# Optimization experiments

Measured on AMD Instinct MI355X. Metric: run time of the kernel, lower is better.

Reference implementation:

```python
import jax, jax.numpy as jnp
import numpy as np

N = 100_000      # nodes
E = 1_600_000    # edges (avg degree 16)
D = 128          # emb_dim == hidden_dim
OUT = 128        # out_dim
NUM_BOND_TYPE = 6
NUM_BOND_DIR = 3


def _xavier(key, fan_in, fan_out, shape):
    a = np.sqrt(6.0 / (fan_in + fan_out)).astype(np.float32)
    return jax.random.uniform(key, shape, jnp.float32, -a, a)


def setup_inputs() -> dict:
    key = jax.random.key(0)
    ks = jax.random.split(key, 12)
    x = jax.random.normal(ks[0], (N, D), jnp.float32)
    edge_index = jax.random.randint(ks[1], (2, E), 0, N)
    edge_attr = jax.random.randint(ks[2], (E, 2), 0, NUM_BOND_DIR)
    # PReLU single learnable slope (torch init 0.25)
    prelu_a = jnp.full((1,), 0.25, jnp.float32)
    # enc_to_dec: Linear(D, D, bias=False), torch default uniform(-1/sqrt(D), 1/sqrt(D))
    s = 1.0 / np.sqrt(D)
    W_enc = jax.random.uniform(ks[3], (D, D), jnp.float32, -s, s)
    # edge embedding tables, xavier_uniform
    emb1 = _xavier(ks[4], NUM_BOND_TYPE, D, (NUM_BOND_TYPE, D))
    emb2 = _xavier(ks[5], NUM_BOND_DIR, D, (NUM_BOND_DIR, D))
    # GIN MLP: Linear(D, 2D) -> ReLU -> Linear(2D, OUT)
    W1 = jax.random.uniform(ks[6], (2 * D, D), jnp.float32, -s, s)
    b1 = jax.random.uniform(ks[7], (2 * D,), jnp.float32, -s, s)
    s2 = 1.0 / np.sqrt(2 * D)
    W2 = jax.random.uniform(ks[8], (OUT, 2 * D), jnp.float32, -s2, s2)
    b2 = jax.random.uniform(ks[9], (OUT,), jnp.float32, -s2, s2)
    return {
        "x": x, "edge_index": edge_index, "edge_attr": edge_attr,
        "prelu_a": prelu_a, "W_enc": W_enc,
        "emb1": emb1, "emb2": emb2,
        "W1": W1, "b1": b1, "W2": W2, "b2": b2,
    }


def reference(x, edge_index, edge_attr, prelu_a, W_enc, emb1, emb2, W1, b1, W2, b2):
    # PReLU then enc_to_dec (no bias)
    h = jnp.where(x >= 0, x, prelu_a * x)          # [N, D]
    h = h @ W_enc.T                                 # [N, D]
    src, dst = edge_index[0], edge_index[1]
    # edge embeddings for real edges
    e_emb = emb1[edge_attr[:, 0]] + emb2[edge_attr[:, 1]]  # [E, D]
    # messages: x_j + edge_attr, scatter-add at dst
    msg = h[src] + e_emb                             # [E, D]
    agg = jax.ops.segment_sum(msg, dst, num_segments=N)    # [N, D]
    # self-loops: appended edge (i, i) with attr [4, 0]
    self_emb = emb1[4] + emb2[0]                     # [D]
    agg = agg + h + self_emb[None, :]
    # GIN update MLP
    hid = jax.nn.relu(agg @ W1.T + b1)               # [N, 2D]
    out = hid @ W2.T + b2                            # [N, OUT]
    return out
```

## Files before the change

kernel.cpp:

```cpp
#include <hip/hip_runtime.h>
#include <hip/hip_bf16.h>

#define DD 128

typedef short bf16x8 __attribute__((ext_vector_type(8)));
typedef float f32x4 __attribute__((ext_vector_type(4)));

__device__ __forceinline__ float bf2f_lo(unsigned int u) {
    union { unsigned int v; float f; } x; x.v = u << 16; return x.f;
}
__device__ __forceinline__ float bf2f_hi(unsigned int u) {
    union { unsigned int v; float f; } x; x.v = u & 0xFFFF0000u; return x.f;
}
__device__ __forceinline__ unsigned short f2bf(float f) {
    union { float f; unsigned int u; } x; x.f = f;
    unsigned int u = x.u;
    unsigned int r = (u + 0x7FFFu + ((u >> 16) & 1u)) >> 16;
    return (unsigned short)r;
}

__global__ __launch_bounds__(256) void wcvt_k(const float* __restrict__ Wenc,
                                              const float* __restrict__ W1,
                                              const float* __restrict__ W2,
                                              unsigned short* __restrict__ wb) {
    int i = (blockIdx.x * 256 + threadIdx.x) * 4;
    if (i >= 81920) return;
    const float* src;
    int off;
    if (i < 16384)      { src = Wenc; off = 0; }
    else if (i < 49152) { src = W1;   off = 16384; }
    else                { src = W2;   off = 49152; }
    float4 v = *(const float4*)&src[i - off];
    ushort4 w;
    w.x = f2bf(v.x); w.y = f2bf(v.y); w.z = f2bf(v.z); w.w = f2bf(v.w);
    *(ushort4*)&wb[i] = w;
}

__global__ __launch_bounds__(256) void gemm1_k(
    const float* __restrict__ Ap, const unsigned short* __restrict__ Wb,
    unsigned short* __restrict__ Hb,
    const float* __restrict__ prelu_a, int M)
{
    const int K = 128;
    const int tid = threadIdx.x;
    const int wid = tid >> 6, lane = tid & 63;
    const float pa = prelu_a[0];

    const int r0 = blockIdx.x * 128 + wid * 32;
    const int rl = lane & 15, kb = (lane >> 4) * 8;

    bf16x8 af[2][4];
    #pragma unroll
    for (int rf = 0; rf < 2; ++rf) {
        int row = r0 + rf * 16 + rl; if (row > M - 1) row = M - 1;
        #pragma unroll
        for (int kf = 0; kf < 4; ++kf) {
            float4 v0 = *(const float4*)&Ap[(size_t)row * K + kf * 32 + kb];
            float4 v1 = *(const float4*)&Ap[(size_t)row * K + kf * 32 + kb + 4];
            v0.x = v0.x >= 0.f ? v0.x : pa * v0.x;
            v0.y = v0.y >= 0.f ? v0.y : pa * v0.y;
            v0.z = v0.z >= 0.f ? v0.z : pa * v0.z;
            v0.w = v0.w >= 0.f ? v0.w : pa * v0.w;
            v1.x = v1.x >= 0.f ? v1.x : pa * v1.x;
            v1.y = v1.y >= 0.f ? v1.y : pa * v1.y;
            v1.z = v1.z >= 0.f ? v1.z : pa * v1.z;
            v1.w = v1.w >= 0.f ? v1.w : pa * v1.w;
            bf16x8 t;
            t[0] = (short)f2bf(v0.x); t[1] = (short)f2bf(v0.y);
            t[2] = (short)f2bf(v0.z); t[3] = (short)f2bf(v0.w);
            t[4] = (short)f2bf(v1.x); t[5] = (short)f2bf(v1.y);
            t[6] = (short)f2bf(v1.z); t[7] = (short)f2bf(v1.w);
            af[rf][kf] = t;
        }
    }

    f32x4 acc[8][2];
    const f32x4 zz = {0.f, 0.f, 0.f, 0.f};
    #pragma unroll
    for (int nt = 0; nt < 8; ++nt) { acc[nt][0] = zz; acc[nt][1] = zz; }

    #pragma unroll
    for (int nt = 0; nt < 8; ++nt) {
        bf16x8 bf[4];
        #pragma unroll
        for (int kf = 0; kf < 4; ++kf)
            bf[kf] = *(const bf16x8*)&Wb[(size_t)(nt * 16 + rl) * K + kf * 32 + kb];
        #pragma unroll
        for (int rf = 0; rf < 2; ++rf)
            #pragma unroll
            for (int kf = 0; kf < 4; ++kf)
                acc[nt][rf] = __builtin_amdgcn_mfma_f32_16x16x32_bf16(af[rf][kf], bf[kf], acc[nt][rf], 0, 0, 0);
    }

    const int rq = (lane >> 4) * 4;
    #pragma unroll
    for (int nt = 0; nt < 8; ++nt) {
        int c = nt * 16 + rl;
        #pragma unroll
        for (int rf = 0; rf < 2; ++rf) {
            int rb = r0 + rf * 16 + rq;
            #pragma unroll
            for (int t = 0; t < 4; ++t) {
                int r = rb + t;
                if (r < M) Hb[(size_t)r * 128 + c] = f2bf(acc[nt][rf][t]);
            }
        }
    }
}

__global__ __launch_bounds__(512) void mlp_k(
    const unsigned short* __restrict__ A,
    const unsigned short* __restrict__ w1b,
    const float* __restrict__ b1,
    const unsigned short* __restrict__ w2b,
    const float* __restrict__ b2,
    float* __restrict__ out, int M)
{
    __shared__ unsigned short W1l[256][136];
    __shared__ unsigned short hidl[128][264];
    unsigned short (*W2l)[264] = (unsigned short (*)[264])&W1l[0][0];

    const int tid = threadIdx.x;
    const int wid = tid >> 6, lane = tid & 63;
    const int rl = lane & 15, kb = (lane >> 4) * 8;
    const int rq = (lane >> 4) * 4;
    const int r0 = blockIdx.x * 128;

    #pragma unroll
    for (int idx = tid; idx < 256 * 16; idx += 512) {
        int n = idx >> 4, kq = idx & 15;
        *(ushort4*)&W1l[n][kq * 8] = *(const ushort4*)&w1b[(size_t)n * 128 + kq * 8];
        *(ushort4*)&W1l[n][kq * 8 + 4] = *(const ushort4*)&w1b[(size_t)n * 128 + kq * 8 + 4];
    }
    bf16x8 af[4];
    {
        int row = r0 + wid * 16 + rl; if (row > M - 1) row = M - 1;
        #pragma unroll
        for (int kf = 0; kf < 4; ++kf)
            af[kf] = *(const bf16x8*)&A[(size_t)row * 128 + kf * 32 + kb];
    }
    __syncthreads();

    f32x4 acc1[16];
    const f32x4 zz = {0.f, 0.f, 0.f, 0.f};
    #pragma unroll
    for (int nt = 0; nt < 16; ++nt) acc1[nt] = zz;
    #pragma unroll
    for (int nt = 0; nt < 16; ++nt) {
        bf16x8 bf[4];
        #pragma unroll
        for (int kf = 0; kf < 4; ++kf)
            bf[kf] = *(const bf16x8*)&W1l[nt * 16 + rl][kf * 32 + kb];
        #pragma unroll
        for (int kf = 0; kf < 4; ++kf)
            acc1[nt] = __builtin_amdgcn_mfma_f32_16x16x32_bf16(af[kf], bf[kf], acc1[nt], 0, 0, 0);
    }
    #pragma unroll
    for (int nt = 0; nt < 16; ++nt) {
        int c = nt * 16 + rl;
        float bi = b1[c];
        #pragma unroll
        for (int t = 0; t < 4; ++t)
            hidl[wid * 16 + rq + t][c] = f2bf(fmaxf(acc1[nt][t] + bi, 0.f));
    }
    __syncthreads();

    #pragma unroll
    for (int idx = tid; idx < 128 * 32; idx += 512) {
        int n = idx >> 5, kq = idx & 31;
        *(ushort4*)&W2l[n][kq * 8] = *(const ushort4*)&w2b[(size_t)n * 256 + kq * 8];
        *(ushort4*)&W2l[n][kq * 8 + 4] = *(const ushort4*)&w2b[(size_t)n * 256 + kq * 8 + 4];
    }
    __syncthreads();

    bf16x8 af2[8];
    #pragma unroll
    for (int kf = 0; kf < 8; ++kf)
        af2[kf] = *(const bf16x8*)&hidl[wid * 16 + rl][kf * 32 + kb];
    f32x4 acc2[8];
    #pragma unroll
    for (int nt = 0; nt < 8; ++nt) acc2[nt] = zz;
    #pragma unroll
    for (int nt = 0; nt < 8; ++nt) {
        bf16x8 bf[8];
        #pragma unroll
        for (int kf = 0; kf < 8; ++kf)
            bf[kf] = *(const bf16x8*)&W2l[nt * 16 + rl][kf * 32 + kb];
        #pragma unroll
        for (int kf = 0; kf < 8; ++kf)
            acc2[nt] = __builtin_amdgcn_mfma_f32_16x16x32_bf16(af2[kf], bf[kf], acc2[nt], 0, 0, 0);
    }
    #pragma unroll
    for (int nt = 0; nt < 8; ++nt) {
        int c = nt * 16 + rl;
        float bi = b2[c];
        #pragma unroll
        for (int t = 0; t < 4; ++t) {
            int r = r0 + wid * 16 + rq + t;
            if (r < M) out[(size_t)r * 128 + c] = acc2[nt][t] + bi;
        }
    }
}


#define SBSH 10
#define SBN  1024
#define NBP 128

__global__ __launch_bounds__(256) void sbhist_k(const int* __restrict__ ei,
                                                int* __restrict__ bh,
                                                int E, int chunk, int nsb) {
    __shared__ int h4[4][128];
    int wid = threadIdx.x >> 6;
    for (int i = threadIdx.x; i < 4 * 128; i += 256) ((int*)h4)[i] = 0;
    __syncthreads();
    int b = blockIdx.x;
    int beg = b * chunk, end = min(E, beg + chunk);
    for (int e = beg + threadIdx.x; e < end; e += 256)
        atomicAdd(&h4[wid][ei[E + e] >> SBSH], 1);
    __syncthreads();
    for (int i = threadIdx.x; i < nsb; i += 256)
        bh[i * NBP + b] = h4[0][i] + h4[1][i] + h4[2][i] + h4[3][i];
}

__global__ __launch_bounds__(1024) void sbscan_k(const int* __restrict__ bh,
                                                 int* __restrict__ bho,
                                                 int ntot, int* __restrict__ offs,
                                                 int M, int E) {
    __shared__ int ws[16];
    int tid = threadIdx.x;
    int ch = (ntot + 1023) / 1024;
    int beg = tid * ch, end = min(ntot, beg + ch);
    int s = 0;
    for (int i = beg; i < end; ++i) s += bh[i];
    int lane = tid & 63, wid = tid >> 6;
    int ss = s;
    #pragma unroll
    for (int o = 1; o < 64; o <<= 1) { int t = __shfl_up(ss, o, 64); if (lane >= o) ss += t; }
    if (lane == 63) ws[wid] = ss;
    __syncthreads();
    if (tid == 0) { int c = 0; for (int w = 0; w < 16; ++w) { int t = ws[w]; ws[w] = c; c += t; } }
    __syncthreads();
    int excl = ss - s + ws[wid];
    for (int i = beg; i < end; ++i) { int t = bh[i]; bho[i] = excl; excl += t; }
    if (tid == 0) offs[M] = E;
}

__global__ __launch_bounds__(256) void part_k(const int* __restrict__ ei,
                                              const int* __restrict__ ea,
                                              const int* __restrict__ bho,
                                              int* __restrict__ rec,
                                              int E, int chunk, int nsb) {
    __shared__ int cur[128];
    int b = blockIdx.x;
    for (int i = threadIdx.x; i < nsb; i += 256) cur[i] = bho[i * NBP + b];
    __syncthreads();
    int beg = b * chunk, end = min(E, beg + chunk);
    for (int e = beg + threadIdx.x; e < end; e += 256) {
        int src = ei[e];
        int dst = ei[E + e];
        int2 aa = *(const int2*)&ea[2 * e];
        int pos = atomicAdd(&cur[dst >> SBSH], 1);
        rec[pos] = src | ((aa.x * 3 + aa.y) << 17) | ((dst & (SBN - 1)) << 21);
    }
}

__global__ __launch_bounds__(1024) void csr_k(const int* __restrict__ rec,
                                              const int* __restrict__ bho,
                                              int* __restrict__ offs,
                                              int* __restrict__ packed,
                                              int nsb, int M, int E) {
    __shared__ int hist[SBN];
    __shared__ int lstart[SBN];
    __shared__ int wsum[16];
    int s = blockIdx.x;
    int t = threadIdx.x;
    int sb0 = bho[s * NBP];
    int sb1 = (s == nsb - 1) ? E : bho[(s + 1) * NBP];
    hist[t] = 0;
    __syncthreads();
    for (int i = sb0 + t; i < sb1; i += 1024)
        atomicAdd(&hist[(rec[i] >> 21) & (SBN - 1)], 1);
    __syncthreads();
    int v = hist[t];
    int lane = t & 63, wid = t >> 6;
    int ss = v;
    #pragma unroll
    for (int o = 1; o < 64; o <<= 1) { int u = __shfl_up(ss, o, 64); if (lane >= o) ss += u; }
    if (lane == 63) wsum[wid] = ss;
    __syncthreads();
    if (t == 0) { int c = 0; for (int w = 0; w < 16; ++w) { int x = wsum[w]; wsum[w] = c; c += x; } }
    __syncthreads();
    int excl = ss - v + wsum[wid];
    lstart[t] = excl;
    int node = (s << SBSH) + t;
    if (node < M) offs[node] = sb0 + excl;
    hist[t] = 0;
    __syncthreads();
    for (int i = sb0 + t; i < sb1; i += 1024) {
        int r = rec[i];
        int dl = (r >> 21) & (SBN - 1);
        int pos = sb0 + lstart[dl] + atomicAdd(&hist[dl], 1);
        packed[pos] = r & 0x1FFFFF;
    }
}

__global__ __launch_bounds__(256) void agg_k(const unsigned short* __restrict__ h,
                                             const int* __restrict__ packed,
                                             const int* __restrict__ offs,
                                             const float* __restrict__ emb1,
                                             const float* __restrict__ emb2,
                                             unsigned int* __restrict__ aggb, int M) {
    __shared__ float emb12[10][DD];
    for (int t = threadIdx.x; t < 10 * DD; t += 256) {
        int c = t >> 7, col = t & 127;
        float v;
        if (c == 9) v = emb1[4 * DD + col] + emb2[col];
        else        v = emb1[(c / 3) * DD + col] + emb2[(c % 3) * DD + col];
        emb12[c][col] = v;
    }
    __syncthreads();
    int wid = threadIdx.x >> 6, lane = threadIdx.x & 63;
    int n = blockIdx.x * 4 + wid;
    if (n >= M) return;
    n = __builtin_amdgcn_readfirstlane(n);
    int c2 = lane * 2;
    int beg = offs[n], end = offs[n + 1];
    unsigned int hn = *(const unsigned int*)&h[(size_t)n * DD + c2];
    float2 se = *(const float2*)&emb12[9][c2];
    float2 acc = {bf2f_lo(hn) + se.x, bf2f_hi(hn) + se.y};
    int e = beg;
    for (; e + 8 <= end; e += 8) {
        int p[8]; unsigned int hv[8]; float2 m[8];
        #pragma unroll
        for (int i = 0; i < 8; ++i) p[i] = packed[e + i];
        #pragma unroll
        for (int i = 0; i < 8; ++i)
            hv[i] = *(const unsigned int*)&h[(size_t)(p[i] & 0x1FFFF) * DD + c2];
        #pragma unroll
        for (int i = 0; i < 8; ++i)
            m[i] = *(const float2*)&emb12[(p[i] >> 17) & 15][c2];
        #pragma unroll
        for (int i = 0; i < 8; ++i) {
            acc.x += bf2f_lo(hv[i]) + m[i].x;
            acc.y += bf2f_hi(hv[i]) + m[i].y;
        }
    }
    if (e + 4 <= end) {
        int p[4]; unsigned int hv[4]; float2 m[4];
        #pragma unroll
        for (int i = 0; i < 4; ++i) p[i] = packed[e + i];
        #pragma unroll
        for (int i = 0; i < 4; ++i)
            hv[i] = *(const unsigned int*)&h[(size_t)(p[i] & 0x1FFFF) * DD + c2];
        #pragma unroll
        for (int i = 0; i < 4; ++i)
            m[i] = *(const float2*)&emb12[(p[i] >> 17) & 15][c2];
        #pragma unroll
        for (int i = 0; i < 4; ++i) {
            acc.x += bf2f_lo(hv[i]) + m[i].x;
            acc.y += bf2f_hi(hv[i]) + m[i].y;
        }
        e += 4;
    }
    for (; e < end; ++e) {
        int p = packed[e];
        unsigned int hv = *(const unsigned int*)&h[(size_t)(p & 0x1FFFF) * DD + c2];
        float2 m = *(const float2*)&emb12[(p >> 17) & 15][c2];
        acc.x += bf2f_lo(hv) + m.x;
        acc.y += bf2f_hi(hv) + m.y;
    }
    aggb[((size_t)n * DD + c2) >> 1] = ((unsigned int)f2bf(acc.y) << 16) | f2bf(acc.x);
}

extern "C" void kernel_launch(void* const* d_in, const int* in_sizes, int n_in,
                              void* d_out, int out_size, void* d_ws, size_t ws_size,
                              hipStream_t stream) {
    const float* x     = (const float*)d_in[0];
    const int*   ei    = (const int*)d_in[1];
    const int*   ea    = (const int*)d_in[2];
    const float* pa    = (const float*)d_in[3];
    const float* Wenc  = (const float*)d_in[4];
    const float* emb1  = (const float*)d_in[5];
    const float* emb2  = (const float*)d_in[6];
    const float* W1    = (const float*)d_in[7];
    const float* b1    = (const float*)d_in[8];
    const float* W2    = (const float*)d_in[9];
    const float* b2    = (const float*)d_in[10];
    float* out = (float*)d_out;

    const int M = in_sizes[0] / DD;
    const int E = in_sizes[1] / 2;
    const int nsb = (M + SBN - 1) >> SBSH;
    const int chunk = (E + NBP - 1) / NBP;

    char* ws = (char*)d_ws;
    size_t o = 0;
    unsigned short* h_bf  = (unsigned short*)(ws + o); o += (size_t)M * DD * 2;
    unsigned int*   aggb  = (unsigned int*)(ws + o);   o += (size_t)M * DD * 2;
    int* rec    = (int*)(ws + o); o += (size_t)E * 4;
    int* packed = (int*)(ws + o); o += (size_t)E * 4;
    int* offs   = (int*)(ws + o); o += (size_t)(M + 1) * 4;
    int* bh     = (int*)(ws + o); o += (size_t)nsb * NBP * 4;
    int* bho    = (int*)(ws + o); o += (size_t)nsb * NBP * 4;
    unsigned short* wb = (unsigned short*)(ws + o); o += 81920 * 2;
    unsigned short* wenc_b = wb;
    unsigned short* w1_b   = wb + 16384;
    unsigned short* w2_b   = wb + 49152;

    dim3 blk(256);

    wcvt_k<<<dim3(80), blk, 0, stream>>>(Wenc, W1, W2, wb);

    sbhist_k<<<dim3(NBP), blk, 0, stream>>>(ei, bh, E, chunk, nsb);
    sbscan_k<<<dim3(1), dim3(1024), 0, stream>>>(bh, bho, nsb * NBP, offs, M, E);
    part_k<<<dim3(NBP), blk, 0, stream>>>(ei, ea, bho, rec, E, chunk, nsb);
    csr_k<<<dim3(nsb), dim3(1024), 0, stream>>>(rec, bho, offs, packed, nsb, M, E);

    gemm1_k<<<dim3((M + 127) / 128), blk, 0, stream>>>(x, wenc_b, h_bf, pa, M);

    agg_k<<<dim3((M + 3) / 4), blk, 0, stream>>>(h_bf, packed, offs, emb1, emb2, aggb, M);

    mlp_k<<<dim3((M + 127) / 128), dim3(512), 0, stream>>>(
        (const unsigned short*)aggb, w1_b, b1, w2_b, b2, out, M);
}
```

Measured before the change: 223.9 us.

## Fuse histogram, weight convert and GEMM1; merge CSR build into aggregation

Merges the destination histogram, the W1/W2 bf16 conversion and the PReLU+enc GEMM into one heterogeneous launch, with Wenc converted inline from fp32 inside each GEMM block. The CSR local sort is fused with aggregation, so each super-bucket block sorts its edges and then aggregates its own nodes without a global offsets array. Super-buckets shrink from 1024 to 128 nodes and the partition block count from 128 to 64. This cuts launches and a global round trip through the offsets array, at the cost of more scan entries, redundant Wenc conversion in every GEMM block, and smaller aggregation grids.

```diff
diff --git a/kernel.cpp b/kernel.cpp
--- a/kernel.cpp
+++ b/kernel.cpp
@@ -19,34 +19,49 @@
     return (unsigned short)r;
 }
 
-__global__ __launch_bounds__(256) void wcvt_k(const float* __restrict__ Wenc,
-                                              const float* __restrict__ W1,
-                                              const float* __restrict__ W2,
-                                              unsigned short* __restrict__ wb) {
-    int i = (blockIdx.x * 256 + threadIdx.x) * 4;
-    if (i >= 81920) return;
-    const float* src;
-    int off;
-    if (i < 16384)      { src = Wenc; off = 0; }
-    else if (i < 49152) { src = W1;   off = 16384; }
-    else                { src = W2;   off = 49152; }
-    float4 v = *(const float4*)&src[i - off];
-    ushort4 w;
-    w.x = f2bf(v.x); w.y = f2bf(v.y); w.z = f2bf(v.z); w.w = f2bf(v.w);
-    *(ushort4*)&wb[i] = w;
-}
-
-__global__ __launch_bounds__(256) void gemm1_k(
-    const float* __restrict__ Ap, const unsigned short* __restrict__ Wb,
-    unsigned short* __restrict__ Hb,
-    const float* __restrict__ prelu_a, int M)
+#define SBSH 7
+#define SBN  128
+#define NBP  64
+#define NSBMAX 800
+
+__global__ __launch_bounds__(256) void gs_k(
+    const float* __restrict__ x, const float* __restrict__ Wenc,
+    const float* __restrict__ W1, const float* __restrict__ W2,
+    const int* __restrict__ ei, const float* __restrict__ prelu_a,
+    unsigned short* __restrict__ Hb, unsigned short* __restrict__ w12b,
+    int* __restrict__ bh, int M, int E, int chunk, int nsb)
 {
+    __shared__ int h4[4][NSBMAX];
+    const int b = blockIdx.x;
+    const int tid = threadIdx.x;
+
+    if (b < NBP) {
+        int wid = tid >> 6;
+        for (int i = tid; i < 4 * NSBMAX; i += 256) ((int*)h4)[i] = 0;
+        __syncthreads();
+        int beg = b * chunk, end = min(E, beg + chunk);
+        for (int e = beg + tid; e < end; e += 256)
+            atomicAdd(&h4[wid][ei[E + e] >> SBSH], 1);
+        __syncthreads();
+        for (int i = tid; i < nsb; i += 256)
+            bh[i * NBP + b] = h4[0][i] + h4[1][i] + h4[2][i] + h4[3][i];
+        return;
+    }
+    if (b < NBP + 64) {
+        int i = ((b - NBP) * 256 + tid) * 4;
+        const float* src = (i < 32768) ? W1 : W2;
+        int off = (i < 32768) ? 0 : 32768;
+        float4 v = *(const float4*)&src[i - off];
+        ushort4 w;
+        w.x = f2bf(v.x); w.y = f2bf(v.y); w.z = f2bf(v.z); w.w = f2bf(v.w);
+        *(ushort4*)&w12b[i] = w;
+        return;
+    }
+
     const int K = 128;
-    const int tid = threadIdx.x;
     const int wid = tid >> 6, lane = tid & 63;
     const float pa = prelu_a[0];
-
-    const int r0 = blockIdx.x * 128 + wid * 32;
+    const int r0 = (b - NBP - 64) * 128 + wid * 32;
     const int rl = lane & 15, kb = (lane >> 4) * 8;
 
     bf16x8 af[2][4];
@@ -55,8 +70,8 @@
         int row = r0 + rf * 16 + rl; if (row > M - 1) row = M - 1;
         #pragma unroll
         for (int kf = 0; kf < 4; ++kf) {
-            float4 v0 = *(const float4*)&Ap[(size_t)row * K + kf * 32 + kb];
-            float4 v1 = *(const float4*)&Ap[(size_t)row * K + kf * 32 + kb + 4];
+            float4 v0 = *(const float4*)&x[(size_t)row * K + kf * 32 + kb];
+            float4 v1 = *(const float4*)&x[(size_t)row * K + kf * 32 + kb + 4];
             v0.x = v0.x >= 0.f ? v0.x : pa * v0.x;
             v0.y = v0.y >= 0.f ? v0.y : pa * v0.y;
             v0.z = v0.z >= 0.f ? v0.z : pa * v0.z;
@@ -83,8 +98,16 @@
     for (int nt = 0; nt < 8; ++nt) {
         bf16x8 bf[4];
         #pragma unroll
-        for (int kf = 0; kf < 4; ++kf)
-            bf[kf] = *(const bf16x8*)&Wb[(size_t)(nt * 16 + rl) * K + kf * 32 + kb];
+        for (int kf = 0; kf < 4; ++kf) {
+            float4 w0 = *(const float4*)&Wenc[(size_t)(nt * 16 + rl) * K + kf * 32 + kb];
+            float4 w1 = *(const float4*)&Wenc[(size_t)(nt * 16 + rl) * K + kf * 32 + kb + 4];
+            bf16x8 t;
+            t[0] = (short)f2bf(w0.x); t[1] = (short)f2bf(w0.y);
+            t[2] = (short)f2bf(w0.z); t[3] = (short)f2bf(w0.w);
+            t[4] = (short)f2bf(w1.x); t[5] = (short)f2bf(w1.y);
+            t[6] = (short)f2bf(w1.z); t[7] = (short)f2bf(w1.w);
+            bf[kf] = t;
+        }
         #pragma unroll
         for (int rf = 0; rf < 2; ++rf)
             #pragma unroll
@@ -105,6 +128,154 @@
                 if (r < M) Hb[(size_t)r * 128 + c] = f2bf(acc[nt][rf][t]);
             }
         }
+    }
+}
+
+__global__ __launch_bounds__(1024) void sbscan_k(const int* __restrict__ bh,
+                                                 int* __restrict__ bho, int ntot) {
+    __shared__ int ws[16];
+    int tid = threadIdx.x;
+    int ch = (ntot + 1023) / 1024;
+    int beg = tid * ch, end = min(ntot, beg + ch);
+    int s = 0;
+    for (int i = beg; i < end; ++i) s += bh[i];
+    int lane = tid & 63, wid = tid >> 6;
+    int ss = s;
+    #pragma unroll
+    for (int o = 1; o < 64; o <<= 1) { int t = __shfl_up(ss, o, 64); if (lane >= o) ss += t; }
+    if (lane == 63) ws[wid] = ss;
+    __syncthreads();
+    if (tid == 0) { int c = 0; for (int w = 0; w < 16; ++w) { int t = ws[w]; ws[w] = c; c += t; } }
+    __syncthreads();
+    int excl = ss - s + ws[wid];
+    for (int i = beg; i < end; ++i) { int t = bh[i]; bho[i] = excl; excl += t; }
+}
+
+__global__ __launch_bounds__(256) void part_k(const int* __restrict__ ei,
+                                              const int* __restrict__ ea,
+                                              const int* __restrict__ bho,
+                                              int* __restrict__ rec,
+                                              int E, int chunk, int nsb) {
+    __shared__ int cur[NSBMAX];
+    int b = blockIdx.x;
+    for (int i = threadIdx.x; i < nsb; i += 256) cur[i] = bho[i * NBP + b];
+    __syncthreads();
+    int beg = b * chunk, end = min(E, beg + chunk);
+    for (int e = beg + threadIdx.x; e < end; e += 256) {
+        int src = ei[e];
+        int dst = ei[E + e];
+        int2 aa = *(const int2*)&ea[2 * e];
+        int pos = atomicAdd(&cur[dst >> SBSH], 1);
+        rec[pos] = src | ((aa.x * 3 + aa.y) << 17) | ((dst & (SBN - 1)) << 21);
+    }
+}
+
+__global__ __launch_bounds__(512) void csragg_k(
+    const unsigned short* __restrict__ h,
+    const int* __restrict__ rec,
+    const int* __restrict__ bho,
+    const float* __restrict__ emb1, const float* __restrict__ emb2,
+    int* __restrict__ packed, unsigned int* __restrict__ aggb,
+    int nsb, int M, int E)
+{
+    __shared__ float emb12[10][DD];
+    __shared__ int hist[SBN];
+    __shared__ int lstart[SBN];
+    __shared__ int wsum[2];
+    const int s = blockIdx.x;
+    const int t = threadIdx.x;
+    const int lane = t & 63, wid = t >> 6;
+
+    for (int i = t; i < 10 * DD; i += 512) {
+        int c = i >> 7, col = i & 127;
+        float v;
+        if (c == 9) v = emb1[4 * DD + col] + emb2[col];
+        else        v = emb1[(c / 3) * DD + col] + emb2[(c % 3) * DD + col];
+        emb12[c][col] = v;
+    }
+    int sb0 = bho[s * NBP];
+    int sb1 = (s == nsb - 1) ? E : bho[(s + 1) * NBP];
+    if (t < SBN) hist[t] = 0;
+    __syncthreads();
+
+    for (int i = sb0 + t; i < sb1; i += 512)
+        atomicAdd(&hist[(rec[i] >> 21) & (SBN - 1)], 1);
+    __syncthreads();
+
+    int v = (t < SBN) ? hist[t] : 0;
+    int ss = v;
+    #pragma unroll
+    for (int o = 1; o < 64; o <<= 1) { int u = __shfl_up(ss, o, 64); if (lane >= o) ss += u; }
+    if (t < SBN && lane == 63) wsum[wid] = ss;
+    __syncthreads();
+    if (t == 0) { int c = 0; for (int w = 0; w < 2; ++w) { int x2 = wsum[w]; wsum[w] = c; c += x2; } }
+    __syncthreads();
+    if (t < SBN) {
+        lstart[t] = ss - v + wsum[wid];
+        hist[t] = 0;
+    }
+    __syncthreads();
+
+    for (int i = sb0 + t; i < sb1; i += 512) {
+        int r = rec[i];
+        int dl = (r >> 21) & (SBN - 1);
+        int pos = sb0 + lstart[dl] + atomicAdd(&hist[dl], 1);
+        packed[pos] = r & 0x1FFFFF;
+    }
+    __syncthreads();
+
+    const int n0 = s << SBSH;
+    const int c2 = lane * 2;
+    for (int k = 0; k < SBN / 8; ++k) {
+        int r = wid + k * 8;
+        int n = n0 + r;
+        if (n >= M) continue;
+        int beg = __builtin_amdgcn_readfirstlane(sb0 + lstart[r]);
+        int end = __builtin_amdgcn_readfirstlane(beg + hist[r]);
+        unsigned int hn = *(const unsigned int*)&h[(size_t)n * DD + c2];
+        float2 acc = {bf2f_lo(hn) + emb12[9][c2], bf2f_hi(hn) + emb12[9][c2 + 1]};
+        int e = beg;
+        for (; e + 8 <= end; e += 8) {
+            int p[8]; unsigned int hv[8]; float2 m[8];
+            #pragma unroll
+            for (int i = 0; i < 8; ++i) p[i] = packed[e + i];
+            #pragma unroll
+            for (int i = 0; i < 8; ++i)
+                hv[i] = *(const unsigned int*)&h[(size_t)(p[i] & 0x1FFFF) * DD + c2];
+            #pragma unroll
+            for (int i = 0; i < 8; ++i)
+                m[i] = *(const float2*)&emb12[(p[i] >> 17) & 15][c2];
+            #pragma unroll
+            for (int i = 0; i < 8; ++i) {
+                acc.x += bf2f_lo(hv[i]) + m[i].x;
+                acc.y += bf2f_hi(hv[i]) + m[i].y;
+            }
+        }
+        if (e + 4 <= end) {
+            int p[4]; unsigned int hv[4]; float2 m[4];
+            #pragma unroll
+            for (int i = 0; i < 4; ++i) p[i] = packed[e + i];
+            #pragma unroll
+            for (int i = 0; i < 4; ++i)
+                hv[i] = *(const unsigned int*)&h[(size_t)(p[i] & 0x1FFFF) * DD + c2];
+            #pragma unroll
+            for (int i = 0; i < 4; ++i)
+                m[i] = *(const float2*)&emb12[(p[i] >> 17) & 15][c2];
+            #pragma unroll
+            for (int i = 0; i < 4; ++i) {
+                acc.x += bf2f_lo(hv[i]) + m[i].x;
+                acc.y += bf2f_hi(hv[i]) + m[i].y;
+            }
+            e += 4;
+        }
+        for (; e < end; ++e) {
+            int p = packed[e];
+            unsigned int hv = *(const unsigned int*)&h[(size_t)(p & 0x1FFFF) * DD + c2];
+            float2 m = *(const float2*)&emb12[(p >> 17) & 15][c2];
+            acc.x += bf2f_lo(hv) + m.x;
+            acc.y += bf2f_hi(hv) + m.y;
+        }
+        aggb[((size_t)n * DD + c2) >> 1] = ((unsigned int)f2bf(acc.y) << 16) | f2bf(acc.x);
     }
 }
 
@@ -200,177 +371,6 @@
             if (r < M) out[(size_t)r * 128 + c] = acc2[nt][t] + bi;
         }
     }
-}
-
-
-#define SBSH 10
-#define SBN  1024
-#define NBP 128
-
-__global__ __launch_bounds__(256) void sbhist_k(const int* __restrict__ ei,
-                                                int* __restrict__ bh,
-                                                int E, int chunk, int nsb) {
-    __shared__ int h4[4][128];
-    int wid = threadIdx.x >> 6;
-    for (int i = threadIdx.x; i < 4 * 128; i += 256) ((int*)h4)[i] = 0;
-    __syncthreads();
-    int b = blockIdx.x;
-    int beg = b * chunk, end = min(E, beg + chunk);
-    for (int e = beg + threadIdx.x; e < end; e += 256)
-        atomicAdd(&h4[wid][ei[E + e] >> SBSH], 1);
-    __syncthreads();
-    for (int i = threadIdx.x; i < nsb; i += 256)
-        bh[i * NBP + b] = h4[0][i] + h4[1][i] + h4[2][i] + h4[3][i];
-}
-
-__global__ __launch_bounds__(1024) void sbscan_k(const int* __restrict__ bh,
-                                                 int* __restrict__ bho,
-                                                 int ntot, int* __restrict__ offs,
-                                                 int M, int E) {
-    __shared__ int ws[16];
-    int tid = threadIdx.x;
-    int ch = (ntot + 1023) / 1024;
-    int beg = tid * ch, end = min(ntot, beg + ch);
-    int s = 0;
-    for (int i = beg; i < end; ++i) s += bh[i];
-    int lane = tid & 63, wid = tid >> 6;
-    int ss = s;
-    #pragma unroll
-    for (int o = 1; o < 64; o <<= 1) { int t = __shfl_up(ss, o, 64); if (lane >= o) ss += t; }
-    if (lane == 63) ws[wid] = ss;
-    __syncthreads();
-    if (tid == 0) { int c = 0; for (int w = 0; w < 16; ++w) { int t = ws[w]; ws[w] = c; c += t; } }
-    __syncthreads();
-    int excl = ss - s + ws[wid];
-    for (int i = beg; i < end; ++i) { int t = bh[i]; bho[i] = excl; excl += t; }
-    if (tid == 0) offs[M] = E;
-}
-
-__global__ __launch_bounds__(256) void part_k(const int* __restrict__ ei,
-                                              const int* __restrict__ ea,
-                                              const int* __restrict__ bho,
-                                              int* __restrict__ rec,
-                                              int E, int chunk, int nsb) {
-    __shared__ int cur[128];
-    int b = blockIdx.x;
-    for (int i = threadIdx.x; i < nsb; i += 256) cur[i] = bho[i * NBP + b];
-    __syncthreads();
-    int beg = b * chunk, end = min(E, beg + chunk);
-    for (int e = beg + threadIdx.x; e < end; e += 256) {
-        int src = ei[e];
-        int dst = ei[E + e];
-        int2 aa = *(const int2*)&ea[2 * e];
-        int pos = atomicAdd(&cur[dst >> SBSH], 1);
-        rec[pos] = src | ((aa.x * 3 + aa.y) << 17) | ((dst & (SBN - 1)) << 21);
-    }
-}
-
-__global__ __launch_bounds__(1024) void csr_k(const int* __restrict__ rec,
-                                              const int* __restrict__ bho,
-                                              int* __restrict__ offs,
-                                              int* __restrict__ packed,
-                                              int nsb, int M, int E) {
-    __shared__ int hist[SBN];
-    __shared__ int lstart[SBN];
-    __shared__ int wsum[16];
-    int s = blockIdx.x;
-    int t = threadIdx.x;
-    int sb0 = bho[s * NBP];
-    int sb1 = (s == nsb - 1) ? E : bho[(s + 1) * NBP];
-    hist[t] = 0;
-    __syncthreads();
-    for (int i = sb0 + t; i < sb1; i += 1024)
-        atomicAdd(&hist[(rec[i] >> 21) & (SBN - 1)], 1);
-    __syncthreads();
-    int v = hist[t];
-    int lane = t & 63, wid = t >> 6;
-    int ss = v;
-    #pragma unroll
-    for (int o = 1; o < 64; o <<= 1) { int u = __shfl_up(ss, o, 64); if (lane >= o) ss += u; }
-    if (lane == 63) wsum[wid] = ss;
-    __syncthreads();
-    if (t == 0) { int c = 0; for (int w = 0; w < 16; ++w) { int x = wsum[w]; wsum[w] = c; c += x; } }
-    __syncthreads();
-    int excl = ss - v + wsum[wid];
-    lstart[t] = excl;
-    int node = (s << SBSH) + t;
-    if (node < M) offs[node] = sb0 + excl;
-    hist[t] = 0;
-    __syncthreads();
-    for (int i = sb0 + t; i < sb1; i += 1024) {
-        int r = rec[i];
-        int dl = (r >> 21) & (SBN - 1);
-        int pos = sb0 + lstart[dl] + atomicAdd(&hist[dl], 1);
-        packed[pos] = r & 0x1FFFFF;
-    }
-}
-
-__global__ __launch_bounds__(256) void agg_k(const unsigned short* __restrict__ h,
-                                             const int* __restrict__ packed,
-                                             const int* __restrict__ offs,
-                                             const float* __restrict__ emb1,
-                                             const float* __restrict__ emb2,
-                                             unsigned int* __restrict__ aggb, int M) {
-    __shared__ float emb12[10][DD];
-    for (int t = threadIdx.x; t < 10 * DD; t += 256) {
-        int c = t >> 7, col = t & 127;
-        float v;
-        if (c == 9) v = emb1[4 * DD + col] + emb2[col];
-        else        v = emb1[(c / 3) * DD + col] + emb2[(c % 3) * DD + col];
-        emb12[c][col] = v;
-    }
-    __syncthreads();
-    int wid = threadIdx.x >> 6, lane = threadIdx.x & 63;
-    int n = blockIdx.x * 4 + wid;
-    if (n >= M) return;
-    n = __builtin_amdgcn_readfirstlane(n);
-    int c2 = lane * 2;
-    int beg = offs[n], end = offs[n + 1];
-    unsigned int hn = *(const unsigned int*)&h[(size_t)n * DD + c2];
-    float2 se = *(const float2*)&emb12[9][c2];
-    float2 acc = {bf2f_lo(hn) + se.x, bf2f_hi(hn) + se.y};
-    int e = beg;
-    for (; e + 8 <= end; e += 8) {
-        int p[8]; unsigned int hv[8]; float2 m[8];
-        #pragma unroll
-        for (int i = 0; i < 8; ++i) p[i] = packed[e + i];
-        #pragma unroll
-        for (int i = 0; i < 8; ++i)
-            hv[i] = *(const unsigned int*)&h[(size_t)(p[i] & 0x1FFFF) * DD + c2];
-        #pragma unroll
-        for (int i = 0; i < 8; ++i)
-            m[i] = *(const float2*)&emb12[(p[i] >> 17) & 15][c2];
-        #pragma unroll
-        for (int i = 0; i < 8; ++i) {
-            acc.x += bf2f_lo(hv[i]) + m[i].x;
-            acc.y += bf2f_hi(hv[i]) + m[i].y;
-        }
-    }
-    if (e + 4 <= end) {
-        int p[4]; unsigned int hv[4]; float2 m[4];
-        #pragma unroll
-        for (int i = 0; i < 4; ++i) p[i] = packed[e + i];
-        #pragma unroll
-        for (int i = 0; i < 4; ++i)
-            hv[i] = *(const unsigned int*)&h[(size_t)(p[i] & 0x1FFFF) * DD + c2];
-        #pragma unroll
-        for (int i = 0; i < 4; ++i)
-            m[i] = *(const float2*)&emb12[(p[i] >> 17) & 15][c2];
-        #pragma unroll
-        for (int i = 0; i < 4; ++i) {
-            acc.x += bf2f_lo(hv[i]) + m[i].x;
-            acc.y += bf2f_hi(hv[i]) + m[i].y;
-        }
-        e += 4;
-    }
-    for (; e < end; ++e) {
-        int p = packed[e];
-        unsigned int hv = *(const unsigned int*)&h[(size_t)(p & 0x1FFFF) * DD + c2];
-        float2 m = *(const float2*)&emb12[(p >> 17) & 15][c2];
-        acc.x += bf2f_lo(hv) + m.x;
-        acc.y += bf2f_hi(hv) + m.y;
-    }
-    aggb[((size_t)n * DD + c2) >> 1] = ((unsigned int)f2bf(acc.y) << 16) | f2bf(acc.x);
 }
 
 extern "C" void kernel_launch(void* const* d_in, const int* in_sizes, int n_in,
@@ -400,27 +400,24 @@
     unsigned int*   aggb  = (unsigned int*)(ws + o);   o += (size_t)M * DD * 2;
     int* rec    = (int*)(ws + o); o += (size_t)E * 4;
     int* packed = (int*)(ws + o); o += (size_t)E * 4;
-    int* offs   = (int*)(ws + o); o += (size_t)(M + 1) * 4;
     int* bh     = (int*)(ws + o); o += (size_t)nsb * NBP * 4;
     int* bho    = (int*)(ws + o); o += (size_t)nsb * NBP * 4;
-    unsigned short* wb = (unsigned short*)(ws + o); o += 81920 * 2;
-    unsigned short* wenc_b = wb;
-    unsigned short* w1_b   = wb + 16384;
-    unsigned short* w2_b   = wb + 49152;
-
-    dim3 blk(256);
-
-    wcvt_k<<<dim3(80), blk, 0, stream>>>(Wenc, W1, W2, wb);
-
-    sbhist_k<<<dim3(NBP), blk, 0, stream>>>(ei, bh, E, chunk, nsb);
-    sbscan_k<<<dim3(1), dim3(1024), 0, stream>>>(bh, bho, nsb * NBP, offs, M, E);
-    part_k<<<dim3(NBP), blk, 0, stream>>>(ei, ea, bho, rec, E, chunk, nsb);
-    csr_k<<<dim3(nsb), dim3(1024), 0, stream>>>(rec, bho, offs, packed, nsb, M, E);
-
-    gemm1_k<<<dim3((M + 127) / 128), blk, 0, stream>>>(x, wenc_b, h_bf, pa, M);
-
-    agg_k<<<dim3((M + 3) / 4), blk, 0, stream>>>(h_bf, packed, offs, emb1, emb2, aggb, M);
-
-    mlp_k<<<dim3((M + 127) / 128), dim3(512), 0, stream>>>(
+    unsigned short* w12b = (unsigned short*)(ws + o); o += 65536 * 2;
+    unsigned short* w1_b = w12b;
+    unsigned short* w2_b = w12b + 32768;
+
+    const int gm = (M + 127) / 128;
+
+    gs_k<<<dim3(NBP + 64 + gm), dim3(256), 0, stream>>>(
+        x, Wenc, W1, W2, ei, pa, h_bf, w12b, bh, M, E, chunk, nsb);
+
+    sbscan_k<<<dim3(1), dim3(1024), 0, stream>>>(bh, bho, nsb * NBP);
+
+    part_k<<<dim3(NBP), dim3(256), 0, stream>>>(ei, ea, bho, rec, E, chunk, nsb);
+
+    csragg_k<<<dim3(nsb), dim3(512), 0, stream>>>(
+        h_bf, rec, bho, emb1, emb2, packed, aggb, nsb, M, E);
+
+    mlp_k<<<dim3(gm), dim3(512), 0, stream>>>(
         (const unsigned short*)aggb, w1_b, b1, w2_b, b2, out, M);
 }
```

Result: slower. 286.8 us (+28.1%).

## Fuse CSR build into aggregation with 128-node superblocks and LDS edge lists

Applied to the files above, without the earlier changes.

Shrinks the destination superblock from 1024 to 128 nodes, so there are about 782 buckets instead of 98. The local counting sort and the gather aggregation now run in one kernel, which keeps each superblock's sorted edge list in shared memory. This removes the separate csr_k pass, the global packed and offs writes and reads, and one launch. The risk is that a single 1024-thread block now handles 128 nodes with 16 waves, and the finer bucketing means larger histograms and more scattered partition writes in sbhist and part_k.

```diff
diff --git a/kernel.cpp b/kernel.cpp
--- a/kernel.cpp
+++ b/kernel.cpp
@@ -18,6 +18,12 @@
     unsigned int r = (u + 0x7FFFu + ((u >> 16) & 1u)) >> 16;
     return (unsigned short)r;
 }
+
+#define SBSH 7
+#define SBN  128
+#define NBP  128
+#define NSBMAX 800
+#define PKCAP 4096
 
 __global__ __launch_bounds__(256) void wcvt_k(const float* __restrict__ Wenc,
                                               const float* __restrict__ W1,
@@ -34,6 +40,61 @@
     ushort4 w;
     w.x = f2bf(v.x); w.y = f2bf(v.y); w.z = f2bf(v.z); w.w = f2bf(v.w);
     *(ushort4*)&wb[i] = w;
+}
+
+__global__ __launch_bounds__(256) void sbhist_k(const int* __restrict__ ei,
+                                                int* __restrict__ bh,
+                                                int E, int chunk, int nsb) {
+    __shared__ int h4[4][NSBMAX];
+    int wid = threadIdx.x >> 6;
+    for (int i = threadIdx.x; i < 4 * NSBMAX; i += 256) ((int*)h4)[i] = 0;
+    __syncthreads();
+    int b = blockIdx.x;
+    int beg = b * chunk, end = min(E, beg + chunk);
+    for (int e = beg + threadIdx.x; e < end; e += 256)
+        atomicAdd(&h4[wid][ei[E + e] >> SBSH], 1);
+    __syncthreads();
+    for (int i = threadIdx.x; i < nsb; i += 256)
+        bh[i * NBP + b] = h4[0][i] + h4[1][i] + h4[2][i] + h4[3][i];
+}
+
+__global__ __launch_bounds__(1024) void sbscan_k(const int* __restrict__ bh,
+                                                 int* __restrict__ bho, int ntot) {
+    __shared__ int ws[16];
+    int tid = threadIdx.x;
+    int ch = (ntot + 1023) / 1024;
+    int beg = tid * ch, end = min(ntot, beg + ch);
+    int s = 0;
+    for (int i = beg; i < end; ++i) s += bh[i];
+    int lane = tid & 63, wid = tid >> 6;
+    int ss = s;
+    #pragma unroll
+    for (int o = 1; o < 64; o <<= 1) { int t = __shfl_up(ss, o, 64); if (lane >= o) ss += t; }
+    if (lane == 63) ws[wid] = ss;
+    __syncthreads();
+    if (tid == 0) { int c = 0; for (int w = 0; w < 16; ++w) { int t = ws[w]; ws[w] = c; c += t; } }
+    __syncthreads();
+    int excl = ss - s + ws[wid];
+    for (int i = beg; i < end; ++i) { int t = bh[i]; bho[i] = excl; excl += t; }
+}
+
+__global__ __launch_bounds__(256) void part_k(const int* __restrict__ ei,
+                                              const int* __restrict__ ea,
+                                              const int* __restrict__ bho,
+                                              int* __restrict__ rec,
+                                              int E, int chunk, int nsb) {
+    __shared__ int cur[NSBMAX];
+    int b = blockIdx.x;
+    for (int i = threadIdx.x; i < nsb; i += 256) cur[i] = bho[i * NBP + b];
+    __syncthreads();
+    int beg = b * chunk, end = min(E, beg + chunk);
+    for (int e = beg + threadIdx.x; e < end; e += 256) {
+        int src = ei[e];
+        int dst = ei[E + e];
+        int2 aa = *(const int2*)&ea[2 * e];
+        int pos = atomicAdd(&cur[dst >> SBSH], 1);
+        rec[pos] = src | ((aa.x * 3 + aa.y) << 17) | ((dst & (SBN - 1)) << 21);
+    }
 }
 
 __global__ __launch_bounds__(256) void gemm1_k(
@@ -108,6 +169,138 @@
     }
 }
 
+__global__ __launch_bounds__(1024) void csragg_k(
+    const unsigned short* __restrict__ h,
+    const int* __restrict__ rec,
+    const int* __restrict__ bho,
+    const float* __restrict__ emb1, const float* __restrict__ emb2,
+    int* __restrict__ packed, unsigned int* __restrict__ aggb,
+    int nsb, int M, int E)
+{
+    __shared__ float emb12[10][DD];
+    __shared__ int hist[SBN];
+    __shared__ int lstart[SBN];
+    __shared__ int wsum[2];
+    __shared__ int pkl[PKCAP];
+    const int s = blockIdx.x;
+    const int t = threadIdx.x;
+    const int lane = t & 63, wid = t >> 6;
+
+    for (int i = t; i < 10 * DD; i += 1024) {
+        int c = i >> 7, col = i & 127;
+        float v;
+        if (c == 9) v = emb1[4 * DD + col] + emb2[col];
+        else        v = emb1[(c / 3) * DD + col] + emb2[(c % 3) * DD + col];
+        emb12[c][col] = v;
+    }
+    int sb0 = bho[s * NBP];
+    int sb1 = (s == nsb - 1) ? E : bho[(s + 1) * NBP];
+    if (t < SBN) hist[t] = 0;
+    __syncthreads();
+
+    const bool inlds = (sb1 - sb0) <= PKCAP;
+
+    for (int i = sb0 + t; i < sb1; i += 1024)
+        atomicAdd(&hist[(rec[i] >> 21) & (SBN - 1)], 1);
+    __syncthreads();
+
+    int v = (t < SBN) ? hist[t] : 0;
+    int ss = v;
+    #pragma unroll
+    for (int o = 1; o < 64; o <<= 1) { int u = __shfl_up(ss, o, 64); if (lane >= o) ss += u; }
+    if (t < SBN && lane == 63) wsum[wid] = ss;
+    __syncthreads();
+    if (t == 0) { int c = 0; for (int w = 0; w < 2; ++w) { int x2 = wsum[w]; wsum[w] = c; c += x2; } }
+    __syncthreads();
+    if (t < SBN) {
+        lstart[t] = ss - v + wsum[wid];
+        hist[t] = 0;
+    }
+    __syncthreads();
+
+    if (inlds) {
+        for (int i = sb0 + t; i < sb1; i += 1024) {
+            int r = rec[i];
+            int dl = (r >> 21) & (SBN - 1);
+            int pos = lstart[dl] + atomicAdd(&hist[dl], 1);
+            pkl[pos] = r & 0x1FFFFF;
+        }
+    } else {
+        for (int i = sb0 + t; i < sb1; i += 1024) {
+            int r = rec[i];
+            int dl = (r >> 21) & (SBN - 1);
+            int pos = sb0 + lstart[dl] + atomicAdd(&hist[dl], 1);
+            packed[pos] = r & 0x1FFFFF;
+        }
+    }
+    __syncthreads();
+
+    const int n0 = s << SBSH;
+    const int c2 = lane * 2;
+    #pragma unroll
+    for (int k = 0; k < SBN / 16; ++k) {
+        int r = wid + k * 16;
+        int n = n0 + r;
+        if (n >= M) continue;
+        int lbeg = lstart[r];
+        int lend = lbeg + hist[r];
+        unsigned int hn = *(const unsigned int*)&h[(size_t)n * DD + c2];
+        float2 acc = {bf2f_lo(hn) + emb12[9][c2], bf2f_hi(hn) + emb12[9][c2 + 1]};
+        if (inlds) {
+            int e = lbeg;
+            for (; e + 8 <= lend; e += 8) {
+                int p[8]; unsigned int hv[8]; float2 m[8];
+                #pragma unroll
+                for (int i = 0; i < 8; ++i) p[i] = pkl[e + i];
+                #pragma unroll
+                for (int i = 0; i < 8; ++i)
+                    hv[i] = *(const unsigned int*)&h[(size_t)(p[i] & 0x1FFFF) * DD + c2];
+                #pragma unroll
+                for (int i = 0; i < 8; ++i)
+                    m[i] = *(const float2*)&emb12[(p[i] >> 17) & 15][c2];
+                #pragma unroll
+                for (int i = 0; i < 8; ++i) {
+                    acc.x += bf2f_lo(hv[i]) + m[i].x;
+                    acc.y += bf2f_hi(hv[i]) + m[i].y;
+                }
+            }
+            for (; e < lend; ++e) {
+                int p = pkl[e];
+                unsigned int hv = *(const unsigned int*)&h[(size_t)(p & 0x1FFFF) * DD + c2];
+                float2 m = *(const float2*)&emb12[(p >> 17) & 15][c2];
+                acc.x += bf2f_lo(hv) + m.x;
+                acc.y += bf2f_hi(hv) + m.y;
+            }
+        } else {
+            int e = sb0 + lbeg, end = sb0 + lend;
+            for (; e + 8 <= end; e += 8) {
+                int p[8]; unsigned int hv[8]; float2 m[8];
+                #pragma unroll
+                for (int i = 0; i < 8; ++i) p[i] = packed[e + i];
+                #pragma unroll
+                for (int i = 0; i < 8; ++i)
+                    hv[i] = *(const unsigned int*)&h[(size_t)(p[i] & 0x1FFFF) * DD + c2];
+                #pragma unroll
+                for (int i = 0; i < 8; ++i)
+                    m[i] = *(const float2*)&emb12[(p[i] >> 17) & 15][c2];
+                #pragma unroll
+                for (int i = 0; i < 8; ++i) {
+                    acc.x += bf2f_lo(hv[i]) + m[i].x;
+                    acc.y += bf2f_hi(hv[i]) + m[i].y;
+                }
+            }
+            for (; e < end; ++e) {
+                int p = packed[e];
+                unsigned int hv = *(const unsigned int*)&h[(size_t)(p & 0x1FFFF) * DD + c2];
+                float2 m = *(const float2*)&emb12[(p >> 17) & 15][c2];
+                acc.x += bf2f_lo(hv) + m.x;
+                acc.y += bf2f_hi(hv) + m.y;
+            }
+        }
+        aggb[((size_t)n * DD + c2) >> 1] = ((unsigned int)f2bf(acc.y) << 16) | f2bf(acc.x);
+    }
+}
+
 __global__ __launch_bounds__(512) void mlp_k(
     const unsigned short* __restrict__ A,
     const unsigned short* __restrict__ w1b,
@@ -200,177 +393,6 @@
             if (r < M) out[(size_t)r * 128 + c] = acc2[nt][t] + bi;
         }
     }
-}
-
-
-#define SBSH 10
-#define SBN  1024
-#define NBP 128
-
-__global__ __launch_bounds__(256) void sbhist_k(const int* __restrict__ ei,
-                                                int* __restrict__ bh,
-                                                int E, int chunk, int nsb) {
-    __shared__ int h4[4][128];
-    int wid = threadIdx.x >> 6;
-    for (int i = threadIdx.x; i < 4 * 128; i += 256) ((int*)h4)[i] = 0;
-    __syncthreads();
-    int b = blockIdx.x;
-    int beg = b * chunk, end = min(E, beg + chunk);
-    for (int e = beg + threadIdx.x; e < end; e += 256)
-        atomicAdd(&h4[wid][ei[E + e] >> SBSH], 1);
-    __syncthreads();
-    for (int i = threadIdx.x; i < nsb; i += 256)
-        bh[i * NBP + b] = h4[0][i] + h4[1][i] + h4[2][i] + h4[3][i];
-}
-
-__global__ __launch_bounds__(1024) void sbscan_k(const int* __restrict__ bh,
-                                                 int* __restrict__ bho,
-                                                 int ntot, int* __restrict__ offs,
-                                                 int M, int E) {
-    __shared__ int ws[16];
-    int tid = threadIdx.x;
-    int ch = (ntot + 1023) / 1024;
-    int beg = tid * ch, end = min(ntot, beg + ch);
-    int s = 0;
-    for (int i = beg; i < end; ++i) s += bh[i];
-    int lane = tid & 63, wid = tid >> 6;
-    int ss = s;
-    #pragma unroll
-    for (int o = 1; o < 64; o <<= 1) { int t = __shfl_up(ss, o, 64); if (lane >= o) ss += t; }
-    if (lane == 63) ws[wid] = ss;
-    __syncthreads();
-    if (tid == 0) { int c = 0; for (int w = 0; w < 16; ++w) { int t = ws[w]; ws[w] = c; c += t; } }
-    __syncthreads();
-    int excl = ss - s + ws[wid];
-    for (int i = beg; i < end; ++i) { int t = bh[i]; bho[i] = excl; excl += t; }
-    if (tid == 0) offs[M] = E;
-}
-
-__global__ __launch_bounds__(256) void part_k(const int* __restrict__ ei,
-                                              const int* __restrict__ ea,
-                                              const int* __restrict__ bho,
-                                              int* __restrict__ rec,
-                                              int E, int chunk, int nsb) {
-    __shared__ int cur[128];
-    int b = blockIdx.x;
-    for (int i = threadIdx.x; i < nsb; i += 256) cur[i] = bho[i * NBP + b];
-    __syncthreads();
-    int beg = b * chunk, end = min(E, beg + chunk);
-    for (int e = beg + threadIdx.x; e < end; e += 256) {
-        int src = ei[e];
-        int dst = ei[E + e];
-        int2 aa = *(const int2*)&ea[2 * e];
-        int pos = atomicAdd(&cur[dst >> SBSH], 1);
-        rec[pos] = src | ((aa.x * 3 + aa.y) << 17) | ((dst & (SBN - 1)) << 21);
-    }
-}
-
-__global__ __launch_bounds__(1024) void csr_k(const int* __restrict__ rec,
-                                              const int* __restrict__ bho,
-                                              int* __restrict__ offs,
-                                              int* __restrict__ packed,
-                                              int nsb, int M, int E) {
-    __shared__ int hist[SBN];
-    __shared__ int lstart[SBN];
-    __shared__ int wsum[16];
-    int s = blockIdx.x;
-    int t = threadIdx.x;
-    int sb0 = bho[s * NBP];
-    int sb1 = (s == nsb - 1) ? E : bho[(s + 1) * NBP];
-    hist[t] = 0;
-    __syncthreads();
-    for (int i = sb0 + t; i < sb1; i += 1024)
-        atomicAdd(&hist[(rec[i] >> 21) & (SBN - 1)], 1);
-    __syncthreads();
-    int v = hist[t];
-    int lane = t & 63, wid = t >> 6;
-    int ss = v;
-    #pragma unroll
-    for (int o = 1; o < 64; o <<= 1) { int u = __shfl_up(ss, o, 64); if (lane >= o) ss += u; }
-    if (lane == 63) wsum[wid] = ss;
-    __syncthreads();
-    if (t == 0) { int c = 0; for (int w = 0; w < 16; ++w) { int x = wsum[w]; wsum[w] = c; c += x; } }
-    __syncthreads();
-    int excl = ss - v + wsum[wid];
-    lstart[t] = excl;
-    int node = (s << SBSH) + t;
-    if (node < M) offs[node] = sb0 + excl;
-    hist[t] = 0;
-    __syncthreads();
-    for (int i = sb0 + t; i < sb1; i += 1024) {
-        int r = rec[i];
-        int dl = (r >> 21) & (SBN - 1);
-        int pos = sb0 + lstart[dl] + atomicAdd(&hist[dl], 1);
-        packed[pos] = r & 0x1FFFFF;
-    }
-}
-
-__global__ __launch_bounds__(256) void agg_k(const unsigned short* __restrict__ h,
-                                             const int* __restrict__ packed,
-                                             const int* __restrict__ offs,
-                                             const float* __restrict__ emb1,
-                                             const float* __restrict__ emb2,
-                                             unsigned int* __restrict__ aggb, int M) {
-    __shared__ float emb12[10][DD];
-    for (int t = threadIdx.x; t < 10 * DD; t += 256) {
-        int c = t >> 7, col = t & 127;
-        float v;
-        if (c == 9) v = emb1[4 * DD + col] + emb2[col];
-        else        v = emb1[(c / 3) * DD + col] + emb2[(c % 3) * DD + col];
-        emb12[c][col] = v;
-    }
-    __syncthreads();
-    int wid = threadIdx.x >> 6, lane = threadIdx.x & 63;
-    int n = blockIdx.x * 4 + wid;
-    if (n >= M) return;
-    n = __builtin_amdgcn_readfirstlane(n);
-    int c2 = lane * 2;
-    int beg = offs[n], end = offs[n + 1];
-    unsigned int hn = *(const unsigned int*)&h[(size_t)n * DD + c2];
-    float2 se = *(const float2*)&emb12[9][c2];
-    float2 acc = {bf2f_lo(hn) + se.x, bf2f_hi(hn) + se.y};
-    int e = beg;
-    for (; e + 8 <= end; e += 8) {
-        int p[8]; unsigned int hv[8]; float2 m[8];
-        #pragma unroll
-        for (int i = 0; i < 8; ++i) p[i] = packed[e + i];
-        #pragma unroll
-        for (int i = 0; i < 8; ++i)
-            hv[i] = *(const unsigned int*)&h[(size_t)(p[i] & 0x1FFFF) * DD + c2];
-        #pragma unroll
-        for (int i = 0; i < 8; ++i)
-            m[i] = *(const float2*)&emb12[(p[i] >> 17) & 15][c2];
-        #pragma unroll
-        for (int i = 0; i < 8; ++i) {
-            acc.x += bf2f_lo(hv[i]) + m[i].x;
-            acc.y += bf2f_hi(hv[i]) + m[i].y;
-        }
-    }
-    if (e + 4 <= end) {
-        int p[4]; unsigned int hv[4]; float2 m[4];
-        #pragma unroll
-        for (int i = 0; i < 4; ++i) p[i] = packed[e + i];
-        #pragma unroll
-        for (int i = 0; i < 4; ++i)
-            hv[i] = *(const unsigned int*)&h[(size_t)(p[i] & 0x1FFFF) * DD + c2];
-        #pragma unroll
-        for (int i = 0; i < 4; ++i)
-            m[i] = *(const float2*)&emb12[(p[i] >> 17) & 15][c2];
-        #pragma unroll
-        for (int i = 0; i < 4; ++i) {
-            acc.x += bf2f_lo(hv[i]) + m[i].x;
-            acc.y += bf2f_hi(hv[i]) + m[i].y;
-        }
-        e += 4;
-    }
-    for (; e < end; ++e) {
-        int p = packed[e];
-        unsigned int hv = *(const unsigned int*)&h[(size_t)(p & 0x1FFFF) * DD + c2];
-        float2 m = *(const float2*)&emb12[(p >> 17) & 15][c2];
-        acc.x += bf2f_lo(hv) + m.x;
-        acc.y += bf2f_hi(hv) + m.y;
-    }
-    aggb[((size_t)n * DD + c2) >> 1] = ((unsigned int)f2bf(acc.y) << 16) | f2bf(acc.x);
 }
 
 extern "C" void kernel_launch(void* const* d_in, const int* in_sizes, int n_in,
@@ -400,7 +422,6 @@
     unsigned int*   aggb  = (unsigned int*)(ws + o);   o += (size_t)M * DD * 2;
     int* rec    = (int*)(ws + o); o += (size_t)E * 4;
     int* packed = (int*)(ws + o); o += (size_t)E * 4;
-    int* offs   = (int*)(ws + o); o += (size_t)(M + 1) * 4;
     int* bh     = (int*)(ws + o); o += (size_t)nsb * NBP * 4;
     int* bho    = (int*)(ws + o); o += (size_t)nsb * NBP * 4;
     unsigned short* wb = (unsigned short*)(ws + o); o += 81920 * 2;
@@ -408,19 +429,20 @@
     unsigned short* w1_b   = wb + 16384;
     unsigned short* w2_b   = wb + 49152;
 
+    const int gm = (M + 127) / 128;
     dim3 blk(256);
 
     wcvt_k<<<dim3(80), blk, 0, stream>>>(Wenc, W1, W2, wb);
 
     sbhist_k<<<dim3(NBP), blk, 0, stream>>>(ei, bh, E, chunk, nsb);
-    sbscan_k<<<dim3(1), dim3(1024), 0, stream>>>(bh, bho, nsb * NBP, offs, M, E);
+    sbscan_k<<<dim3(1), dim3(1024), 0, stream>>>(bh, bho, nsb * NBP);
     part_k<<<dim3(NBP), blk, 0, stream>>>(ei, ea, bho, rec, E, chunk, nsb);
-    csr_k<<<dim3(nsb), dim3(1024), 0, stream>>>(rec, bho, offs, packed, nsb, M, E);
-
-    gemm1_k<<<dim3((M + 127) / 128), blk, 0, stream>>>(x, wenc_b, h_bf, pa, M);
-
-    agg_k<<<dim3((M + 3) / 4), blk, 0, stream>>>(h_bf, packed, offs, emb1, emb2, aggb, M);
-
-    mlp_k<<<dim3((M + 127) / 128), dim3(512), 0, stream>>>(
+
+    gemm1_k<<<dim3(gm), blk, 0, stream>>>(x, wenc_b, h_bf, pa, M);
+
+    csragg_k<<<dim3(nsb), dim3(1024), 0, stream>>>(
+        h_bf, rec, bho, emb1, emb2, packed, aggb, nsb, M, E);
+
+    mlp_k<<<dim3(gm), dim3(512), 0, stream>>>(
         (const unsigned short*)aggb, w1_b, b1, w2_b, b2, out, M);
 }
```

New measurement: 356.3 us. 1.59x slower.
